# Performance work log

Measured on AMD Instinct MI355X. Metric: run time of the kernel, lower is better.

## Reference

```python
import jax, jax.numpy as jnp
import numpy as np

N, IN_F, OUT_F = 1024, 256, 1024

def setup_inputs() -> dict:
    key = jax.random.key(0)
    k1, k2 = jax.random.split(key)
    x = jax.random.normal(k1, (N, IN_F), dtype=jnp.float32)
    centres = jax.random.normal(k2, (OUT_F, IN_F), dtype=jnp.float32)  # normal_(0,1) init
    log_sigmas = jnp.zeros((OUT_F,), dtype=jnp.float32)  # constant_(0) init
    return {"x": x, "centres": centres, "log_sigmas": log_sigmas}

def reference(x, centres, log_sigmas):
    # diff: (N, out_features, in_features) broadcast, matching torch expand
    diff = x[:, None, :] - centres[None, :, :]
    # Euclidean distance then per-centre sigma scaling: (N, out_features)
    distances = jnp.sqrt(jnp.sum(diff * diff, axis=-1)) / jnp.exp(log_sigmas)[None, :]
    # gaussian basis function: exp(-0.5 * d^2)
    return jnp.exp(-0.5 * distances * distances)
```

## Files before the change

kernel.cpp:

```cpp
#include <hip/hip_runtime.h>
#include <math.h>

#define N_ROWS 1024
#define K_FEAT 256
#define M_OUT  1024

#define TILE 64
#define BK   64
#define LDS_STRIDE 68

__global__ __launch_bounds__(256) void rbf_kernel(
    const float* __restrict__ x,
    const float* __restrict__ centres,
    const float* __restrict__ log_sigmas,
    float* __restrict__ out)
{
    __shared__ float xs[BK][LDS_STRIDE];
    __shared__ float cs[BK][LDS_STRIDE];

    const int tid = threadIdx.x;
    const int row_base = blockIdx.y * TILE;
    const int col_base = blockIdx.x * TILE;

    const int r0 = (tid & 15) * 4;
    const int c0 = (tid >> 4) * 4;

    float acc[4][4] = {};

    for (int kc = 0; kc < K_FEAT; kc += BK) {
        #pragma unroll
        for (int l = 0; l < 4; ++l) {
            const int f   = tid + l * 256;
            const int row = f >> 4;
            const int k0  = (f & 15) * 4;
            const float4 xv = *(const float4*)(x       + (size_t)(row_base + row) * K_FEAT + kc + k0);
            const float4 cv = *(const float4*)(centres + (size_t)(col_base + row) * K_FEAT + kc + k0);
            xs[k0 + 0][row] = xv.x; xs[k0 + 1][row] = xv.y;
            xs[k0 + 2][row] = xv.z; xs[k0 + 3][row] = xv.w;
            cs[k0 + 0][row] = cv.x; cs[k0 + 1][row] = cv.y;
            cs[k0 + 2][row] = cv.z; cs[k0 + 3][row] = cv.w;
        }
        __syncthreads();

        #pragma unroll
        for (int k = 0; k < BK; ++k) {
            const float4 xv = *(const float4*)&xs[k][r0];
            const float4 cv = *(const float4*)&cs[k][c0];
            const float xr[4] = {xv.x, xv.y, xv.z, xv.w};
            const float cr[4] = {cv.x, cv.y, cv.z, cv.w};
            #pragma unroll
            for (int i = 0; i < 4; ++i) {
                #pragma unroll
                for (int j = 0; j < 4; ++j) {
                    const float d = xr[i] - cr[j];
                    acc[i][j] = fmaf(d, d, acc[i][j]);
                }
            }
        }
        __syncthreads();
    }

    float inv2sig[4];
    #pragma unroll
    for (int j = 0; j < 4; ++j)
        inv2sig[j] = __expf(-2.0f * log_sigmas[col_base + c0 + j]);

    #pragma unroll
    for (int i = 0; i < 4; ++i) {
        float4 v;
        v.x = expf(-0.5f * acc[i][0] * inv2sig[0]);
        v.y = expf(-0.5f * acc[i][1] * inv2sig[1]);
        v.z = expf(-0.5f * acc[i][2] * inv2sig[2]);
        v.w = expf(-0.5f * acc[i][3] * inv2sig[3]);
        *(float4*)(out + (size_t)(row_base + r0 + i) * M_OUT + col_base + c0) = v;
    }
}

extern "C" void kernel_launch(void* const* d_in, const int* in_sizes, int n_in,
                              void* d_out, int out_size, void* d_ws, size_t ws_size,
                              hipStream_t stream) {
    const float* x  = (const float*)d_in[0];
    const float* c  = (const float*)d_in[1];
    const float* ls = (const float*)d_in[2];
    float* out = (float*)d_out;

    dim3 grid(M_OUT / TILE, N_ROWS / TILE);
    rbf_kernel<<<grid, dim3(256), 0, stream>>>(x, c, ls, out);
}
```

Before: 77.34 us.

## Compute RBF distances via norm expansion with bf16 MFMA matrix cores

```diff
diff --git a/kernel.cpp b/kernel.cpp
--- a/kernel.cpp
+++ b/kernel.cpp
@@ -1,78 +1,111 @@
 #include <hip/hip_runtime.h>
 #include <math.h>
 
-#define N_ROWS 1024
 #define K_FEAT 256
 #define M_OUT  1024
+#define N_ROWS 1024
 
-#define TILE 64
-#define BK   64
-#define LDS_STRIDE 68
+#define TM 64
+#define TN 32
+#define LSTR 264
 
-__global__ __launch_bounds__(256) void rbf_kernel(
+typedef short bf16x8 __attribute__((ext_vector_type(8)));
+typedef float f32x4  __attribute__((ext_vector_type(4)));
+
+__global__ __launch_bounds__(256, 2) void rbf_mfma(
     const float* __restrict__ x,
     const float* __restrict__ centres,
     const float* __restrict__ log_sigmas,
     float* __restrict__ out)
 {
-    __shared__ float xs[BK][LDS_STRIDE];
-    __shared__ float cs[BK][LDS_STRIDE];
+    __shared__ unsigned short xs[TM * LSTR];
+    __shared__ unsigned short cs[TN * LSTR];
+    __shared__ float nx[TM];
+    __shared__ float nc[TN];
 
-    const int tid = threadIdx.x;
-    const int row_base = blockIdx.y * TILE;
-    const int col_base = blockIdx.x * TILE;
+    const int tid  = threadIdx.x;
+    const int lane = tid & 63;
+    const int wave = tid >> 6;
+    const int row_base = blockIdx.y * TM;
+    const int col_base = blockIdx.x * TN;
 
-    const int r0 = (tid & 15) * 4;
-    const int c0 = (tid >> 4) * 4;
+    #pragma unroll
+    for (int l = 0; l < 12; ++l) {
+        const int  li    = (l < 8) ? l : (l - 8);
+        const int  chunk = tid + li * 256;
+        const int  row   = chunk >> 5;
+        const int  k0    = (chunk & 31) * 8;
+        const float* src = (l < 8)
+            ? (x       + (size_t)(row_base + row) * K_FEAT + k0)
+            : (centres + (size_t)(col_base + row) * K_FEAT + k0);
+        const float4 v0 = ((const float4*)src)[0];
+        const float4 v1 = ((const float4*)src)[1];
+        uint4 p;
+        p.x = (__float_as_uint(v0.x) >> 16) | (__float_as_uint(v0.y) & 0xffff0000u);
+        p.y = (__float_as_uint(v0.z) >> 16) | (__float_as_uint(v0.w) & 0xffff0000u);
+        p.z = (__float_as_uint(v1.x) >> 16) | (__float_as_uint(v1.y) & 0xffff0000u);
+        p.w = (__float_as_uint(v1.z) >> 16) | (__float_as_uint(v1.w) & 0xffff0000u);
+        unsigned short* dst = (l < 8) ? &xs[row * LSTR + k0] : &cs[row * LSTR + k0];
+        *(uint4*)dst = p;
+    }
+    __syncthreads();
 
-    float acc[4][4] = {};
-
-    for (int kc = 0; kc < K_FEAT; kc += BK) {
+    if (tid < TM + TN) {
+        const unsigned short* src = (tid < TM) ? &xs[tid * LSTR] : &cs[(tid - TM) * LSTR];
+        float s0 = 0.f, s1 = 0.f, s2 = 0.f, s3 = 0.f;
         #pragma unroll
-        for (int l = 0; l < 4; ++l) {
-            const int f   = tid + l * 256;
-            const int row = f >> 4;
-            const int k0  = (f & 15) * 4;
-            const float4 xv = *(const float4*)(x       + (size_t)(row_base + row) * K_FEAT + kc + k0);
-            const float4 cv = *(const float4*)(centres + (size_t)(col_base + row) * K_FEAT + kc + k0);
-            xs[k0 + 0][row] = xv.x; xs[k0 + 1][row] = xv.y;
-            xs[k0 + 2][row] = xv.z; xs[k0 + 3][row] = xv.w;
-            cs[k0 + 0][row] = cv.x; cs[k0 + 1][row] = cv.y;
-            cs[k0 + 2][row] = cv.z; cs[k0 + 3][row] = cv.w;
+        for (int k = 0; k < K_FEAT; k += 8) {
+            const uint4 q = *(const uint4*)(src + k);
+            const float f0 = __uint_as_float(q.x << 16);
+            const float f1 = __uint_as_float(q.x & 0xffff0000u);
+            const float f2 = __uint_as_float(q.y << 16);
+            const float f3 = __uint_as_float(q.y & 0xffff0000u);
+            const float f4 = __uint_as_float(q.z << 16);
+            const float f5 = __uint_as_float(q.z & 0xffff0000u);
+            const float f6 = __uint_as_float(q.w << 16);
+            const float f7 = __uint_as_float(q.w & 0xffff0000u);
+            s0 = fmaf(f0, f0, s0); s1 = fmaf(f1, f1, s1);
+            s2 = fmaf(f2, f2, s2); s3 = fmaf(f3, f3, s3);
+            s0 = fmaf(f4, f4, s0); s1 = fmaf(f5, f5, s1);
+            s2 = fmaf(f6, f6, s2); s3 = fmaf(f7, f7, s3);
         }
-        __syncthreads();
-
-        #pragma unroll
-        for (int k = 0; k < BK; ++k) {
-            const float4 xv = *(const float4*)&xs[k][r0];
-            const float4 cv = *(const float4*)&cs[k][c0];
-            const float xr[4] = {xv.x, xv.y, xv.z, xv.w};
-            const float cr[4] = {cv.x, cv.y, cv.z, cv.w};
-            #pragma unroll
-            for (int i = 0; i < 4; ++i) {
-                #pragma unroll
-                for (int j = 0; j < 4; ++j) {
-                    const float d = xr[i] - cr[j];
-                    acc[i][j] = fmaf(d, d, acc[i][j]);
-                }
-            }
-        }
-        __syncthreads();
+        const float s = (s0 + s1) + (s2 + s3);
+        if (tid < TM) nx[tid] = s; else nc[tid - TM] = s;
     }
 
-    float inv2sig[4];
+    const int m    = lane & 15;
+    const int quad = lane >> 4;
+    const int row_slab = wave * 16;
+    f32x4 acc0 = {0.f, 0.f, 0.f, 0.f};
+    f32x4 acc1 = {0.f, 0.f, 0.f, 0.f};
+    const unsigned short* ap  = &xs[(row_slab + m) * LSTR + quad * 8];
+    const unsigned short* bp0 = &cs[ m       * LSTR + quad * 8];
+    const unsigned short* bp1 = &cs[(16 + m) * LSTR + quad * 8];
     #pragma unroll
-    for (int j = 0; j < 4; ++j)
-        inv2sig[j] = __expf(-2.0f * log_sigmas[col_base + c0 + j]);
+    for (int kk = 0; kk < 8; ++kk) {
+        const bf16x8 a  = *(const bf16x8*)(ap  + kk * 32);
+        const bf16x8 b0 = *(const bf16x8*)(bp0 + kk * 32);
+        const bf16x8 b1 = *(const bf16x8*)(bp1 + kk * 32);
+        acc0 = __builtin_amdgcn_mfma_f32_16x16x32_bf16(a, b0, acc0, 0, 0, 0);
+        acc1 = __builtin_amdgcn_mfma_f32_16x16x32_bf16(a, b1, acc1, 0, 0, 0);
+    }
+    __syncthreads();
 
+    const int col0 = col_base + m;
+    const int col1 = col_base + 16 + m;
+    const float i2s0 = __expf(-2.0f * log_sigmas[col0]);
+    const float i2s1 = __expf(-2.0f * log_sigmas[col1]);
+    const float ncv0 = nc[m];
+    const float ncv1 = nc[16 + m];
     #pragma unroll
     for (int i = 0; i < 4; ++i) {
-        float4 v;
-        v.x = expf(-0.5f * acc[i][0] * inv2sig[0]);
-        v.y = expf(-0.5f * acc[i][1] * inv2sig[1]);
-        v.z = expf(-0.5f * acc[i][2] * inv2sig[2]);
-        v.w = expf(-0.5f * acc[i][3] * inv2sig[3]);
-        *(float4*)(out + (size_t)(row_base + r0 + i) * M_OUT + col_base + c0) = v;
+        const int r = row_slab + quad * 4 + i;
+        const float nxv = nx[r];
+        const float d0 = nxv + ncv0 - 2.0f * acc0[i];
+        const float d1 = nxv + ncv1 - 2.0f * acc1[i];
+        float* o = out + (size_t)(row_base + r) * M_OUT;
+        o[col0] = __expf(-0.5f * d0 * i2s0);
+        o[col1] = __expf(-0.5f * d1 * i2s1);
     }
 }
 
@@ -84,6 +117,6 @@
     const float* ls = (const float*)d_in[2];
     float* out = (float*)d_out;
 
-    dim3 grid(M_OUT / TILE, N_ROWS / TILE);
-    rbf_kernel<<<grid, dim3(256), 0, stream>>>(x, c, ls, out);
+    dim3 grid(M_OUT / TN, N_ROWS / TM);
+    rbf_mfma<<<grid, dim3(256), 0, stream>>>(x, c, ls, out);
 }
```

New measurement: 62.38 us (median of 2 runs). 19.3% less time.
